# Kernel optimization log

Measured on AMD Instinct MI355X. Metric: run time of the kernel, lower is better.

Reference implementation:

```python
import jax, jax.numpy as jnp
import numpy as np

N, E, D, T, B, OUT = 20000, 80000, 768, 4, 3, 768
SCALE = 0.02


def _layer_norm(x, g, b):
    mu = jnp.mean(x, axis=-1, keepdims=True)
    var = jnp.var(x, axis=-1, keepdims=True)
    return (x - mu) / jnp.sqrt(var + 1e-5) * g + b


def _typed_linear(x, etype, bases, coeff):
    # DGL TypedLinear with basis regularizer: W[t] = sum_b coeff[t,b] * bases[b]
    # computed as 3 shared GEMMs + per-edge weighted sum (avoids [E,D,D] gather).
    c = coeff[etype]  # [E, B]
    y = c[:, 0:1] * (x @ bases[0])
    for bb in range(1, bases.shape[0]):
        y = y + c[:, bb:bb + 1] * (x @ bases[bb])
    return y


def _time_encode(t, freq, phase):
    return jnp.cos(t[:, None] * freq[None, :] + phase[None, :])


def _segment_softmax(scores, seg, n):
    m = jax.ops.segment_max(scores, seg, num_segments=n)
    m = jnp.where(jnp.isfinite(m), m, 0.0)  # empty segments -> -inf guard
    e = jnp.exp(scores - m[seg])
    den = jax.ops.segment_sum(e, seg, num_segments=n)[seg]
    return e / jnp.where(den == 0, 1.0, den)


def _forward(h, etime_hete, first_etime_homo, second_etime_homo, w_src, w_dst,
             ln_g, ln_b, src_bases, src_coeff, dst_bases, dst_coeff,
             user_bases, user_coeff, lin_w, lin_b, time_freq, time_phase,
             src_hete, dst_hete, first_etype_hete, src_homo, dst_homo,
             first_etype_homo, second_etype_homo, n_nodes):
    inv_sqrt_d = 1.0 / jnp.sqrt(jnp.asarray(768.0, h.dtype))
    n_src = h @ w_src.T  # src_weight (no bias)
    n_dst = h @ w_dst.T  # dst_weight (no bias)

    # --- heterogeneous edges ---
    sf = n_src[src_hete]
    df = n_dst[dst_hete]
    hete_src = jax.nn.relu(_typed_linear(_layer_norm(sf, ln_g, ln_b), first_etype_hete, src_bases, src_coeff))
    msg_h = _time_encode(etime_hete, time_freq, time_phase) + hete_src
    e_h = jnp.sum(msg_h * df, axis=1) * inv_sqrt_d
    a_h = _segment_softmax(e_h, dst_hete, n_nodes)
    h_hete = jax.ops.segment_sum(a_h[:, None] * msg_h, dst_hete, num_segments=n_nodes)

    # --- homogeneous edges ---
    sf = n_src[src_homo]
    df = n_dst[dst_homo]
    dst_feat = jax.nn.relu(_typed_linear(_layer_norm(df, ln_g, ln_b), first_etype_homo, dst_bases, dst_coeff))
    homo_feat = jax.nn.relu(_typed_linear(_layer_norm(sf, ln_g, ln_b), second_etype_homo, user_bases, user_coeff))
    t_homo = jnp.maximum(first_etime_homo, second_etime_homo)
    msg_o = _time_encode(t_homo, time_freq, time_phase) + homo_feat
    e_o = jnp.sum(msg_o * dst_feat, axis=1) * inv_sqrt_d
    a_o = _segment_softmax(e_o, dst_homo, n_nodes)
    h_homo = jax.ops.segment_sum(a_o[:, None] * msg_o, dst_homo, num_segments=n_nodes)

    n = jnp.concatenate([h_hete, h_homo], axis=-1)  # [N, 2D]
    z = jax.nn.relu(n @ lin_w.T + lin_b)
    zn = jnp.linalg.norm(z, axis=1, keepdims=True)
    return z / jnp.where(zn == 0, 1.0, zn)


def setup_inputs() -> dict:
    key = jax.random.key(0)
    ks = jax.random.split(key, 24)
    inp = {
        'h': jax.random.normal(ks[0], (N, D), jnp.float32),
        'etime_hete': jax.random.uniform(ks[1], (E,), jnp.float32),
        'first_etime_homo': jax.random.uniform(ks[2], (E,), jnp.float32),
        'second_etime_homo': jax.random.uniform(ks[3], (E,), jnp.float32),
        'w_src': jax.random.normal(ks[4], (D, D), jnp.float32) * SCALE,
        'w_dst': jax.random.normal(ks[5], (D, D), jnp.float32) * SCALE,
        'ln_g': jnp.ones((D,), jnp.float32),
        'ln_b': jnp.zeros((D,), jnp.float32),
        'src_bases': jax.random.normal(ks[6], (B, D, D), jnp.float32) * SCALE,
        'src_coeff': jax.random.normal(ks[7], (T, B), jnp.float32),
        'dst_bases': jax.random.normal(ks[8], (B, D, D), jnp.float32) * SCALE,
        'dst_coeff': jax.random.normal(ks[9], (T, B), jnp.float32),
        'user_bases': jax.random.normal(ks[10], (B, D, D), jnp.float32) * SCALE,
        'user_coeff': jax.random.normal(ks[11], (T, B), jnp.float32),
        'lin_w': jax.random.normal(ks[12], (OUT, 2 * D), jnp.float32) * SCALE,
        'lin_b': jnp.zeros((OUT,), jnp.float32),
        'time_freq': jnp.asarray(1.0 / 10 ** np.linspace(0, 9, D), jnp.float32),
        'time_phase': jnp.zeros((D,), jnp.float32),
        'src_hete': jax.random.randint(ks[13], (E,), 0, N, jnp.int32),
        'dst_hete': jax.random.randint(ks[14], (E,), 0, N, jnp.int32),
        'first_etype_hete': jax.random.randint(ks[15], (E,), 0, T, jnp.int32),
        'src_homo': jax.random.randint(ks[16], (E,), 0, N, jnp.int32),
        'dst_homo': jax.random.randint(ks[17], (E,), 0, N, jnp.int32),
        'first_etype_homo': jax.random.randint(ks[18], (E,), 0, T, jnp.int32),
        'second_etype_homo': jax.random.randint(ks[19], (E,), 0, T, jnp.int32),
        'num_nodes': N,
    }
    return inp


def reference(h, etime_hete, first_etime_homo, second_etime_homo, w_src, w_dst,
              ln_g, ln_b, src_bases, src_coeff, dst_bases, dst_coeff,
              user_bases, user_coeff, lin_w, lin_b, time_freq, time_phase,
              src_hete, dst_hete, first_etype_hete, src_homo, dst_homo,
              first_etype_homo, second_etype_homo, num_nodes):
    return _forward(h, etime_hete, first_etime_homo, second_etime_homo, w_src,
                    w_dst, ln_g, ln_b, src_bases, src_coeff, dst_bases,
                    dst_coeff, user_bases, user_coeff, lin_w, lin_b,
                    time_freq, time_phase, src_hete, dst_hete,
                    first_etype_hete, src_homo, dst_homo, first_etype_homo,
                    second_etype_homo, num_nodes)
```

## Files before the change

kernel.cpp:

```cpp
#include <hip/hip_runtime.h>
#include <hip/hip_bf16.h>
#include <stdint.h>

#define D 768
#define INV_SQRT_D 0.03608439182435161269f

static void* g_scratch = nullptr;
#define SCRATCH_BYTES ((size_t)600 * 1024 * 1024)

__attribute__((constructor))
static void _alloc_scratch() {
    if (hipMalloc(&g_scratch, SCRATCH_BYTES) != hipSuccess) g_scratch = nullptr;
}

static inline int cdiv(int a, int b) { return (a + b - 1) / b; }

typedef __attribute__((ext_vector_type(8))) short bf16x8;
typedef __attribute__((ext_vector_type(4))) float f32x4;

__device__ __forceinline__ unsigned short f2b(float f) {
    union { float f; unsigned u; } c; c.f = f;
    unsigned r = c.u + 0x7FFF + ((c.u >> 16) & 1);
    return (unsigned short)(r >> 16);
}
__device__ __forceinline__ float b2f(unsigned short u) {
    union { unsigned u; float f; } c; c.u = (unsigned)u << 16;
    return c.f;
}

__device__ __forceinline__ float block_reduce_sum(float v) {
#pragma unroll
    for (int off = 32; off > 0; off >>= 1) v += __shfl_down(v, off, 64);
    __shared__ float sm[4];
    int lane = threadIdx.x & 63, w = threadIdx.x >> 6;
    __syncthreads();
    if (lane == 0) sm[w] = v;
    __syncthreads();
    return (sm[0] + sm[1]) + (sm[2] + sm[3]);
}

template <bool CONCAT, bool BF16C, bool RELU_BIAS>
__global__ __launch_bounds__(256) void mfma_gemm(
    const unsigned short* __restrict__ A1, const unsigned short* __restrict__ A2,
    int lda, int ksplit,
    const unsigned short* __restrict__ B, int ldb,
    void* __restrict__ Cv, int ldc,
    const float* __restrict__ bias,
    int M, int K)
{
    __shared__ unsigned short As[128 * 32];
    __shared__ unsigned short Bs[128 * 32];
    const int tid = threadIdx.x;
    const int wv = tid >> 6, lane = tid & 63;
    const int m0 = blockIdx.y * 128, n0 = blockIdx.x * 128;
    const int wm = (wv >> 1) << 6;
    const int wn = (wv & 1) << 6;
    const int fr = lane & 15;
    const int fq = lane >> 4;

    f32x4 acc[4][4] = {};

    for (int k0 = 0; k0 < K; k0 += 32) {
        const unsigned short* Asrc = A1;
        int kk = k0;
        if (CONCAT && k0 >= ksplit) { Asrc = A2; kk = k0 - ksplit; }
#pragma unroll
        for (int j = 0; j < 2; ++j) {
            int idx = j * 256 + tid;
            int row = idx >> 2, cb = (idx & 3) << 3;
            int am = m0 + row; if (am > M - 1) am = M - 1;
            const unsigned short* ga = Asrc + (size_t)am * lda + kk + cb;
            char* la = (char*)As + (size_t)(j * 256 + wv * 64) * 16;
            __builtin_amdgcn_global_load_lds(
                (const __attribute__((address_space(1))) unsigned int*)ga,
                (__attribute__((address_space(3))) unsigned int*)la, 16, 0, 0);
            const unsigned short* gb = B + (size_t)(n0 + row) * ldb + k0 + cb;
            char* lb = (char*)Bs + (size_t)(j * 256 + wv * 64) * 16;
            __builtin_amdgcn_global_load_lds(
                (const __attribute__((address_space(1))) unsigned int*)gb,
                (__attribute__((address_space(3))) unsigned int*)lb, 16, 0, 0);
        }
        __syncthreads();

        bf16x8 af[4], bfv[4];
#pragma unroll
        for (int i = 0; i < 4; ++i) {
            af[i]  = *(const bf16x8*)&As[(wm + i * 16 + fr) * 32 + fq * 8];
            bfv[i] = *(const bf16x8*)&Bs[(wn + i * 16 + fr) * 32 + fq * 8];
        }
#pragma unroll
        for (int mi = 0; mi < 4; ++mi)
#pragma unroll
            for (int ni = 0; ni < 4; ++ni)
                acc[mi][ni] = __builtin_amdgcn_mfma_f32_16x16x32_bf16(
                    af[mi], bfv[ni], acc[mi][ni], 0, 0, 0);
        __syncthreads();
    }

#pragma unroll
    for (int mi = 0; mi < 4; ++mi) {
#pragma unroll
        for (int r = 0; r < 4; ++r) {
            int m = m0 + wm + mi * 16 + fq * 4 + r;
            if (m >= M) continue;
#pragma unroll
            for (int ni = 0; ni < 4; ++ni) {
                int n = n0 + wn + ni * 16 + fr;
                float v = acc[mi][ni][r];
                if (RELU_BIAS) v = fmaxf(v + bias[n], 0.f);
                if (BF16C) ((unsigned short*)Cv)[(size_t)m * ldc + n] = f2b(v);
                else       ((float*)Cv)[(size_t)m * ldc + n] = v;
            }
        }
    }
}

__global__ void f32_to_bf16_kernel(const float* __restrict__ in,
                                   unsigned short* __restrict__ out, int n4) {
    int i = blockIdx.x * 256 + threadIdx.x;
    if (i >= n4) return;
    float4 v = *reinterpret_cast<const float4*>(in + (size_t)i * 4);
    ushort4 o;
    o.x = f2b(v.x); o.y = f2b(v.y); o.z = f2b(v.z); o.w = f2b(v.w);
    *reinterpret_cast<ushort4*>(out + (size_t)i * 4) = o;
}

__global__ __launch_bounds__(256) void transpose_f32_to_bf16(
    const float* __restrict__ in, unsigned short* __restrict__ out) {
    const float* src = in + (size_t)blockIdx.z * D * D;
    unsigned short* dst = out + (size_t)blockIdx.z * D * D;
    __shared__ float tile[32][33];
    int bx = blockIdx.x * 32, by = blockIdx.y * 32;
    int tx = threadIdx.x & 31, ty = threadIdx.x >> 5;
#pragma unroll
    for (int i = 0; i < 32; i += 8)
        tile[ty + i][tx] = src[(size_t)(by + ty + i) * D + bx + tx];
    __syncthreads();
#pragma unroll
    for (int i = 0; i < 32; i += 8)
        dst[(size_t)(bx + ty + i) * D + by + tx] = f2b(tile[tx][ty + i]);
}

__global__ __launch_bounds__(256) void ln_bf16_kernel(
    unsigned short* __restrict__ x, int ld,
    const float* __restrict__ g, const float* __restrict__ b)
{
    unsigned short* r = x + (size_t)blockIdx.x * ld;
    int t = threadIdx.x;
    float v0 = b2f(r[t]), v1 = b2f(r[t + 256]), v2 = b2f(r[t + 512]);
    float s = block_reduce_sum(v0 + v1 + v2);
    float mu = s * (1.f / 768.f);
    float d0 = v0 - mu, d1 = v1 - mu, d2 = v2 - mu;
    float q = block_reduce_sum(d0 * d0 + d1 * d1 + d2 * d2);
    float rstd = 1.f / sqrtf(q * (1.f / 768.f) + 1e-5f);
    r[t]       = f2b(d0 * rstd * g[t]       + b[t]);
    r[t + 256] = f2b(d1 * rstd * g[t + 256] + b[t + 256]);
    r[t + 512] = f2b(d2 * rstd * g[t + 512] + b[t + 512]);
}

__global__ __launch_bounds__(256) void score_hete_kernel(
    const unsigned short* __restrict__ P, int ldp,
    const unsigned short* __restrict__ nd, int ldn,
    const float* __restrict__ coeff, const float* __restrict__ etime,
    const int* __restrict__ src, const int* __restrict__ dst, const int* __restrict__ et,
    const float* __restrict__ freq, const float* __restrict__ phase,
    float* __restrict__ esc)
{
    int e = blockIdx.x;
    int s = src[e], d = dst[e], ty = et[e];
    float c0 = coeff[ty * 3 + 0], c1 = coeff[ty * 3 + 1], c2 = coeff[ty * 3 + 2];
    float tv = etime[e];
    const unsigned short* ps = P + (size_t)s * ldp;
    const unsigned short* pd = nd + (size_t)d * ldn;
    float acc = 0.f;
    int j = threadIdx.x;
#pragma unroll
    for (int r = 0; r < 3; ++r, j += 256) {
        float y = c0 * b2f(ps[j]) + c1 * b2f(ps[j + D]) + c2 * b2f(ps[j + 2 * D]);
        float m = __cosf(tv * freq[j] + phase[j]) + fmaxf(y, 0.f);
        acc += m * b2f(pd[j]);
    }
    acc = block_reduce_sum(acc);
    if (threadIdx.x == 0) esc[e] = acc * INV_SQRT_D;
}

__global__ __launch_bounds__(256) void score_homo_kernel(
    const unsigned short* __restrict__ Pd, int ldpd,
    const unsigned short* __restrict__ Pu, int ldpu,
    const float* __restrict__ dcoeff, const float* __restrict__ ucoeff,
    const float* __restrict__ t1, const float* __restrict__ t2,
    const int* __restrict__ src, const int* __restrict__ dst,
    const int* __restrict__ et1, const int* __restrict__ et2,
    const float* __restrict__ freq, const float* __restrict__ phase,
    float* __restrict__ esc)
{
    int e = blockIdx.x;
    int s = src[e], d = dst[e];
    int ta = et1[e], tb = et2[e];
    float d0 = dcoeff[ta * 3 + 0], d1 = dcoeff[ta * 3 + 1], d2 = dcoeff[ta * 3 + 2];
    float u0 = ucoeff[tb * 3 + 0], u1 = ucoeff[tb * 3 + 1], u2 = ucoeff[tb * 3 + 2];
    float tv = fmaxf(t1[e], t2[e]);
    const unsigned short* pu = Pu + (size_t)s * ldpu;
    const unsigned short* pd = Pd + (size_t)d * ldpd;
    float acc = 0.f;
    int j = threadIdx.x;
#pragma unroll
    for (int r = 0; r < 3; ++r, j += 256) {
        float m  = __cosf(tv * freq[j] + phase[j])
                 + fmaxf(u0 * b2f(pu[j]) + u1 * b2f(pu[j + D]) + u2 * b2f(pu[j + 2 * D]), 0.f);
        float df = fmaxf(d0 * b2f(pd[j]) + d1 * b2f(pd[j + D]) + d2 * b2f(pd[j + 2 * D]), 0.f);
        acc += m * df;
    }
    acc = block_reduce_sum(acc);
    if (threadIdx.x == 0) esc[e] = acc * INV_SQRT_D;
}

__global__ void zero_int_kernel(int* __restrict__ p, int n) {
    int i = blockIdx.x * 256 + threadIdx.x;
    if (i < n) p[i] = 0;
}

__global__ void count_kernel(const int* __restrict__ dst, int* __restrict__ cnt, int E) {
    int e = blockIdx.x * 256 + threadIdx.x;
    if (e < E) atomicAdd(&cnt[dst[e]], 1);
}

__global__ __launch_bounds__(1024) void scan_kernel(
    const int* __restrict__ cnt, int* __restrict__ offs, int n)
{
    __shared__ int tmp[1024];
    __shared__ int carry;
    int tid = threadIdx.x;
    if (tid == 0) carry = 0;
    __syncthreads();
    for (int base = 0; base < n; base += 1024) {
        int idx = base + tid;
        int v = (idx < n) ? cnt[idx] : 0;
        tmp[tid] = v;
        __syncthreads();
        for (int off = 1; off < 1024; off <<= 1) {
            int t = (tid >= off) ? tmp[tid - off] : 0;
            __syncthreads();
            tmp[tid] += t;
            __syncthreads();
        }
        int inc = tmp[tid];
        int c = carry;
        if (idx < n) offs[idx] = c + inc - v;
        __syncthreads();
        if (tid == 0) carry = c + tmp[1023];
        __syncthreads();
    }
    if (tid == 0) offs[n] = carry;
}

__global__ void scatter_kernel(const int* __restrict__ dst, const int* __restrict__ offs,
                               int* __restrict__ cur, int* __restrict__ list, int E) {
    int e = blockIdx.x * 256 + threadIdx.x;
    if (e < E) {
        int d = dst[e];
        int pos = offs[d] + atomicAdd(&cur[d], 1);
        list[pos] = e;
    }
}

__global__ void seg_softmax_kernel(const int* __restrict__ offs, const int* __restrict__ list,
                                   float* __restrict__ score, int n) {
    int v = blockIdx.x * 256 + threadIdx.x;
    if (v >= n) return;
    int a = offs[v], b = offs[v + 1];
    if (a == b) return;
    float m = -INFINITY;
    for (int i = a; i < b; i++) m = fmaxf(m, score[list[i]]);
    float den = 0.f;
    for (int i = a; i < b; i++) den += expf(score[list[i]] - m);
    float inv = 1.f / den;
    for (int i = a; i < b; i++) { int e = list[i]; score[e] = expf(score[e] - m) * inv; }
}

__global__ __launch_bounds__(256) void agg_hete_kernel(
    const int* __restrict__ offs, const int* __restrict__ list,
    const float* __restrict__ a,
    const unsigned short* __restrict__ P, int ldp,
    const float* __restrict__ coeff, const float* __restrict__ etime,
    const int* __restrict__ src, const int* __restrict__ et,
    const float* __restrict__ freq, const float* __restrict__ phase,
    unsigned short* __restrict__ out)
{
    int v = blockIdx.x;
    int t = threadIdx.x;
    float f0 = freq[t], f1 = freq[t + 256], f2 = freq[t + 512];
    float p0 = phase[t], p1 = phase[t + 256], p2 = phase[t + 512];
    float a0 = 0.f, a1 = 0.f, a2 = 0.f;
    for (int i = offs[v]; i < offs[v + 1]; ++i) {
        int e = list[i];
        int s = src[e], ty = et[e];
        float w = a[e];
        float c0 = coeff[ty * 3 + 0], c1 = coeff[ty * 3 + 1], c2 = coeff[ty * 3 + 2];
        float tv = etime[e];
        const unsigned short* ps = P + (size_t)s * ldp;
        float y0 = c0 * b2f(ps[t])       + c1 * b2f(ps[t + D])       + c2 * b2f(ps[t + 2 * D]);
        float y1 = c0 * b2f(ps[t + 256]) + c1 * b2f(ps[t + 256 + D]) + c2 * b2f(ps[t + 256 + 2 * D]);
        float y2 = c0 * b2f(ps[t + 512]) + c1 * b2f(ps[t + 512 + D]) + c2 * b2f(ps[t + 512 + 2 * D]);
        a0 += w * (__cosf(tv * f0 + p0) + fmaxf(y0, 0.f));
        a1 += w * (__cosf(tv * f1 + p1) + fmaxf(y1, 0.f));
        a2 += w * (__cosf(tv * f2 + p2) + fmaxf(y2, 0.f));
    }
    unsigned short* o = out + (size_t)v * D;
    o[t] = f2b(a0); o[t + 256] = f2b(a1); o[t + 512] = f2b(a2);
}

__global__ __launch_bounds__(256) void agg_homo_kernel(
    const int* __restrict__ offs, const int* __restrict__ list,
    const float* __restrict__ a,
    const unsigned short* __restrict__ Pu, int ldpu,
    const float* __restrict__ ucoeff,
    const float* __restrict__ t1, const float* __restrict__ t2,
    const int* __restrict__ src, const int* __restrict__ et2,
    const float* __restrict__ freq, const float* __restrict__ phase,
    unsigned short* __restrict__ out)
{
    int v = blockIdx.x;
    int t = threadIdx.x;
    float f0 = freq[t], f1 = freq[t + 256], f2 = freq[t + 512];
    float p0 = phase[t], p1 = phase[t + 256], p2 = phase[t + 512];
    float a0 = 0.f, a1 = 0.f, a2 = 0.f;
    for (int i = offs[v]; i < offs[v + 1]; ++i) {
        int e = list[i];
        int s = src[e], tb = et2[e];
        float w = a[e];
        float u0 = ucoeff[tb * 3 + 0], u1 = ucoeff[tb * 3 + 1], u2 = ucoeff[tb * 3 + 2];
        float tv = fmaxf(t1[e], t2[e]);
        const unsigned short* pu = Pu + (size_t)s * ldpu;
        float y0 = u0 * b2f(pu[t])       + u1 * b2f(pu[t + D])       + u2 * b2f(pu[t + 2 * D]);
        float y1 = u0 * b2f(pu[t + 256]) + u1 * b2f(pu[t + 256 + D]) + u2 * b2f(pu[t + 256 + 2 * D]);
        float y2 = u0 * b2f(pu[t + 512]) + u1 * b2f(pu[t + 512 + D]) + u2 * b2f(pu[t + 512 + 2 * D]);
        a0 += w * (__cosf(tv * f0 + p0) + fmaxf(y0, 0.f));
        a1 += w * (__cosf(tv * f1 + p1) + fmaxf(y1, 0.f));
        a2 += w * (__cosf(tv * f2 + p2) + fmaxf(y2, 0.f));
    }
    unsigned short* o = out + (size_t)v * D;
    o[t] = f2b(a0); o[t + 256] = f2b(a1); o[t + 512] = f2b(a2);
}

__global__ __launch_bounds__(256) void normalize_kernel(
    const float* __restrict__ z, float* __restrict__ out)
{
    const float* x = z + (size_t)blockIdx.x * D;
    int t = threadIdx.x;
    float v0 = x[t], v1 = x[t + 256], v2 = x[t + 512];
    float s = block_reduce_sum(v0 * v0 + v1 * v1 + v2 * v2);
    float nrm = sqrtf(s);
    float inv = (nrm == 0.f) ? 1.f : 1.f / nrm;
    float* o = out + (size_t)blockIdx.x * D;
    o[t] = v0 * inv; o[t + 256] = v1 * inv; o[t + 512] = v2 * inv;
}

__global__ void fill_f32_kernel(float* __restrict__ p, float v, int n) {
    int i = blockIdx.x * 256 + threadIdx.x;
    if (i < n) p[i] = v;
}

extern "C" void kernel_launch(void* const* d_in, const int* in_sizes, int n_in,
                              void* d_out, int out_size, void* d_ws, size_t ws_size,
                              hipStream_t stream)
{
    const float* h          = (const float*)d_in[0];
    const float* etime_hete = (const float*)d_in[1];
    const float* t1_homo    = (const float*)d_in[2];
    const float* t2_homo    = (const float*)d_in[3];
    const float* w_src      = (const float*)d_in[4];
    const float* w_dst      = (const float*)d_in[5];
    const float* ln_g       = (const float*)d_in[6];
    const float* ln_b       = (const float*)d_in[7];
    const float* src_bases  = (const float*)d_in[8];
    const float* src_coeff  = (const float*)d_in[9];
    const float* dst_bases  = (const float*)d_in[10];
    const float* dst_coeff  = (const float*)d_in[11];
    const float* user_bases = (const float*)d_in[12];
    const float* user_coeff = (const float*)d_in[13];
    const float* lin_w      = (const float*)d_in[14];
    const float* lin_b      = (const float*)d_in[15];
    const float* time_freq  = (const float*)d_in[16];
    const float* time_phase = (const float*)d_in[17];
    const int* src_hete = (const int*)d_in[18];
    const int* dst_hete = (const int*)d_in[19];
    const int* et_hete  = (const int*)d_in[20];
    const int* src_homo = (const int*)d_in[21];
    const int* dst_homo = (const int*)d_in[22];
    const int* et1_homo = (const int*)d_in[23];
    const int* et2_homo = (const int*)d_in[24];

    const int N = in_sizes[0] / D;
    const int E = in_sizes[1];

    const size_t szST  = (size_t)N * 1536 * 2;
    const size_t szPSU = (size_t)N * 4608 * 2;
    const size_t szPD  = (size_t)N * 2304 * 2;
    const size_t szVb  = (size_t)N * D * 2;
    const size_t szW   = (size_t)D * D * 2;
    size_t need = szST + szPSU + szPD + 3 * szVb + 2 * szW + 2 * szW
                + 6 * szW + 3 * szW
                + (size_t)E * 4 + (size_t)N * 4
                + (((size_t)(N + 1) * 4 + 255) & ~(size_t)255) + (size_t)E * 4 + 4096;

    char* base;
    if (ws_size >= need) base = (char*)d_ws;
    else if (g_scratch)  base = (char*)g_scratch;
    else {
        fill_f32_kernel<<<cdiv(out_size, 256), 256, 0, stream>>>(
            (float*)d_out, 1000.0f + (float)(ws_size >> 20), out_size);
        return;
    }

    char* p = base;
    auto carve = [&](size_t bytes) { char* r = p; p += (bytes + 255) & ~(size_t)255; return r; };
    unsigned short* STb = (unsigned short*)carve(szST);
    unsigned short* PSU = (unsigned short*)carve(szPSU);
    unsigned short* PD  = (unsigned short*)carve(szPD);
    unsigned short* hb  = (unsigned short*)carve(szVb);
    unsigned short* hAb = (unsigned short*)carve(szVb);
    unsigned short* hOb = (unsigned short*)carve(szVb);
    unsigned short* wsb = (unsigned short*)carve(2 * szW);
    unsigned short* lwb = (unsigned short*)carve(2 * szW);
    unsigned short* suT = (unsigned short*)carve(6 * szW);
    unsigned short* dstT = (unsigned short*)carve(3 * szW);
    float* esc = (float*)carve((size_t)E * 4);
    int* cnt   = (int*)carve((size_t)N * 4);
    int* offs  = (int*)carve((size_t)(N + 1) * 4);
    int* list  = (int*)carve((size_t)E * 4);
    float* z   = (float*)PSU;

    unsigned short* Sb = STb;
    unsigned short* Tb = STb + 768;
    unsigned short* Psrc  = PSU;
    unsigned short* Puser = PSU + 2304;

    const int eb = cdiv(E, 256), nb = cdiv(N, 256);
    const int MB = cdiv(N, 128);
    dim3 g_proj(12, MB);
    dim3 g_psu(36, MB);
    dim3 g_pd(18, MB);
    dim3 g_fin(6, MB);
    dim3 tr_grid(24, 24, 3);

    f32_to_bf16_kernel<<<cdiv(N * D / 4, 256), 256, 0, stream>>>(h, hb, N * D / 4);
    f32_to_bf16_kernel<<<cdiv(D * D / 4, 256), 256, 0, stream>>>(w_src, wsb, D * D / 4);
    f32_to_bf16_kernel<<<cdiv(D * D / 4, 256), 256, 0, stream>>>(w_dst, wsb + (size_t)D * D, D * D / 4);
    f32_to_bf16_kernel<<<cdiv(D * 2 * D / 4, 256), 256, 0, stream>>>(lin_w, lwb, D * 2 * D / 4);
    transpose_f32_to_bf16<<<tr_grid, 256, 0, stream>>>(src_bases, suT);
    transpose_f32_to_bf16<<<tr_grid, 256, 0, stream>>>(user_bases, suT + (size_t)3 * D * D);
    transpose_f32_to_bf16<<<tr_grid, 256, 0, stream>>>(dst_bases, dstT);

    mfma_gemm<false, true, false><<<g_proj, 256, 0, stream>>>(
        hb, hb, D, D, wsb, D, STb, 1536, nullptr, N, D);
    ln_bf16_kernel<<<N, 256, 0, stream>>>(Sb, 1536, ln_g, ln_b);

    mfma_gemm<false, true, false><<<g_psu, 256, 0, stream>>>(
        Sb, Sb, 1536, D, suT, D, PSU, 4608, nullptr, N, D);

    zero_int_kernel<<<nb, 256, 0, stream>>>(cnt, N);
    count_kernel<<<eb, 256, 0, stream>>>(dst_hete, cnt, E);
    scan_kernel<<<1, 1024, 0, stream>>>(cnt, offs, N);
    zero_int_kernel<<<nb, 256, 0, stream>>>(cnt, N);
    scatter_kernel<<<eb, 256, 0, stream>>>(dst_hete, offs, cnt, list, E);

    score_hete_kernel<<<E, 256, 0, stream>>>(Psrc, 4608, Tb, 1536, src_coeff, etime_hete,
                                             src_hete, dst_hete, et_hete,
                                             time_freq, time_phase, esc);
    seg_softmax_kernel<<<nb, 256, 0, stream>>>(offs, list, esc, N);
    agg_hete_kernel<<<N, 256, 0, stream>>>(offs, list, esc, Psrc, 4608, src_coeff, etime_hete,
                                           src_hete, et_hete, time_freq, time_phase, hAb);

    ln_bf16_kernel<<<N, 256, 0, stream>>>(Tb, 1536, ln_g, ln_b);
    mfma_gemm<false, true, false><<<g_pd, 256, 0, stream>>>(
        Tb, Tb, 1536, D, dstT, D, PD, 2304, nullptr, N, D);

    zero_int_kernel<<<nb, 256, 0, stream>>>(cnt, N);
    count_kernel<<<eb, 256, 0, stream>>>(dst_homo, cnt, E);
    scan_kernel<<<1, 1024, 0, stream>>>(cnt, offs, N);
    zero_int_kernel<<<nb, 256, 0, stream>>>(cnt, N);
    scatter_kernel<<<eb, 256, 0, stream>>>(dst_homo, offs, cnt, list, E);

    score_homo_kernel<<<E, 256, 0, stream>>>(PD, 2304, Puser, 4608, dst_coeff, user_coeff,
                                             t1_homo, t2_homo, src_homo, dst_homo,
                                             et1_homo, et2_homo, time_freq, time_phase, esc);
    seg_softmax_kernel<<<nb, 256, 0, stream>>>(offs, list, esc, N);
    agg_homo_kernel<<<N, 256, 0, stream>>>(offs, list, esc, Puser, 4608, user_coeff,
                                           t1_homo, t2_homo, src_homo, et2_homo,
                                           time_freq, time_phase, hOb);

    mfma_gemm<true, false, true><<<g_fin, 256, 0, stream>>>(
        hAb, hOb, D, D, lwb, 2 * D, z, D, lin_b, N, 2 * D);
    normalize_kernel<<<N, 256, 0, stream>>>(z, (float*)d_out);
}
```

Before: 1.170 ms.

## Precombine basis weights per edge type and fuse ReLU into projection GEMMs

```diff
diff --git a/kernel.cpp b/kernel.cpp
--- a/kernel.cpp
+++ b/kernel.cpp
@@ -39,7 +39,7 @@
     return (sm[0] + sm[1]) + (sm[2] + sm[3]);
 }
 
-template <bool CONCAT, bool BF16C, bool RELU_BIAS>
+template <bool CONCAT, bool BF16C, bool RELU, bool BIAS>
 __global__ __launch_bounds__(256) void mfma_gemm(
     const unsigned short* __restrict__ A1, const unsigned short* __restrict__ A2,
     int lda, int ksplit,
@@ -107,7 +107,8 @@
             for (int ni = 0; ni < 4; ++ni) {
                 int n = n0 + wn + ni * 16 + fr;
                 float v = acc[mi][ni][r];
-                if (RELU_BIAS) v = fmaxf(v + bias[n], 0.f);
+                if (BIAS) v += bias[n];
+                if (RELU) v = fmaxf(v, 0.f);
                 if (BF16C) ((unsigned short*)Cv)[(size_t)m * ldc + n] = f2b(v);
                 else       ((float*)Cv)[(size_t)m * ldc + n] = v;
             }
@@ -125,20 +126,25 @@
     *reinterpret_cast<ushort4*>(out + (size_t)i * 4) = o;
 }
 
-__global__ __launch_bounds__(256) void transpose_f32_to_bf16(
-    const float* __restrict__ in, unsigned short* __restrict__ out) {
-    const float* src = in + (size_t)blockIdx.z * D * D;
-    unsigned short* dst = out + (size_t)blockIdx.z * D * D;
+__global__ __launch_bounds__(256) void combine_transpose_kernel(
+    const float* __restrict__ in, const float* __restrict__ coeff,
+    unsigned short* __restrict__ out) {
+    int t = blockIdx.z;
+    float c0 = coeff[t * 3 + 0], c1 = coeff[t * 3 + 1], c2 = coeff[t * 3 + 2];
     __shared__ float tile[32][33];
     int bx = blockIdx.x * 32, by = blockIdx.y * 32;
     int tx = threadIdx.x & 31, ty = threadIdx.x >> 5;
 #pragma unroll
+    for (int i = 0; i < 32; i += 8) {
+        size_t idx = (size_t)(by + ty + i) * D + bx + tx;
+        tile[ty + i][tx] = c0 * in[idx] + c1 * in[idx + (size_t)D * D]
+                         + c2 * in[idx + (size_t)2 * D * D];
+    }
+    __syncthreads();
+    unsigned short* o = out + (size_t)t * D * D;
+#pragma unroll
     for (int i = 0; i < 32; i += 8)
-        tile[ty + i][tx] = src[(size_t)(by + ty + i) * D + bx + tx];
-    __syncthreads();
-#pragma unroll
-    for (int i = 0; i < 32; i += 8)
-        dst[(size_t)(bx + ty + i) * D + by + tx] = f2b(tile[tx][ty + i]);
+        o[(size_t)(bx + ty + i) * D + by + tx] = f2b(tile[tx][ty + i]);
 }
 
 __global__ __launch_bounds__(256) void ln_bf16_kernel(
@@ -161,58 +167,85 @@
 __global__ __launch_bounds__(256) void score_hete_kernel(
     const unsigned short* __restrict__ P, int ldp,
     const unsigned short* __restrict__ nd, int ldn,
-    const float* __restrict__ coeff, const float* __restrict__ etime,
+    const float* __restrict__ etime,
     const int* __restrict__ src, const int* __restrict__ dst, const int* __restrict__ et,
     const float* __restrict__ freq, const float* __restrict__ phase,
-    float* __restrict__ esc)
-{
-    int e = blockIdx.x;
+    float* __restrict__ esc, int E)
+{
+    int e = blockIdx.x * 4 + (threadIdx.x >> 6);
+    if (e >= E) return;
+    int l = threadIdx.x & 63;
     int s = src[e], d = dst[e], ty = et[e];
-    float c0 = coeff[ty * 3 + 0], c1 = coeff[ty * 3 + 1], c2 = coeff[ty * 3 + 2];
     float tv = etime[e];
-    const unsigned short* ps = P + (size_t)s * ldp;
+    const unsigned short* ps = P + (size_t)s * ldp + ty * D;
     const unsigned short* pd = nd + (size_t)d * ldn;
     float acc = 0.f;
-    int j = threadIdx.x;
-#pragma unroll
-    for (int r = 0; r < 3; ++r, j += 256) {
-        float y = c0 * b2f(ps[j]) + c1 * b2f(ps[j + D]) + c2 * b2f(ps[j + 2 * D]);
-        float m = __cosf(tv * freq[j] + phase[j]) + fmaxf(y, 0.f);
-        acc += m * b2f(pd[j]);
-    }
-    acc = block_reduce_sum(acc);
-    if (threadIdx.x == 0) esc[e] = acc * INV_SQRT_D;
+    {
+        bf16x8 a = *(const bf16x8*)(ps + l * 8);
+        bf16x8 b = *(const bf16x8*)(pd + l * 8);
+#pragma unroll
+        for (int q = 0; q < 8; ++q) {
+            int j = l * 8 + q;
+            float m = __cosf(tv * freq[j] + phase[j]) + b2f((unsigned short)a[q]);
+            acc += m * b2f((unsigned short)b[q]);
+        }
+    }
+    if (l < 32) {
+        bf16x8 a = *(const bf16x8*)(ps + 512 + l * 8);
+        bf16x8 b = *(const bf16x8*)(pd + 512 + l * 8);
+#pragma unroll
+        for (int q = 0; q < 8; ++q) {
+            int j = 512 + l * 8 + q;
+            float m = __cosf(tv * freq[j] + phase[j]) + b2f((unsigned short)a[q]);
+            acc += m * b2f((unsigned short)b[q]);
+        }
+    }
+#pragma unroll
+    for (int off = 32; off > 0; off >>= 1) acc += __shfl_down(acc, off, 64);
+    if (l == 0) esc[e] = acc * INV_SQRT_D;
 }
 
 __global__ __launch_bounds__(256) void score_homo_kernel(
     const unsigned short* __restrict__ Pd, int ldpd,
     const unsigned short* __restrict__ Pu, int ldpu,
-    const float* __restrict__ dcoeff, const float* __restrict__ ucoeff,
     const float* __restrict__ t1, const float* __restrict__ t2,
     const int* __restrict__ src, const int* __restrict__ dst,
     const int* __restrict__ et1, const int* __restrict__ et2,
     const float* __restrict__ freq, const float* __restrict__ phase,
-    float* __restrict__ esc)
-{
-    int e = blockIdx.x;
+    float* __restrict__ esc, int E)
+{
+    int e = blockIdx.x * 4 + (threadIdx.x >> 6);
+    if (e >= E) return;
+    int l = threadIdx.x & 63;
     int s = src[e], d = dst[e];
     int ta = et1[e], tb = et2[e];
-    float d0 = dcoeff[ta * 3 + 0], d1 = dcoeff[ta * 3 + 1], d2 = dcoeff[ta * 3 + 2];
-    float u0 = ucoeff[tb * 3 + 0], u1 = ucoeff[tb * 3 + 1], u2 = ucoeff[tb * 3 + 2];
     float tv = fmaxf(t1[e], t2[e]);
-    const unsigned short* pu = Pu + (size_t)s * ldpu;
-    const unsigned short* pd = Pd + (size_t)d * ldpd;
+    const unsigned short* pu = Pu + (size_t)s * ldpu + tb * D;
+    const unsigned short* pd = Pd + (size_t)d * ldpd + ta * D;
     float acc = 0.f;
-    int j = threadIdx.x;
-#pragma unroll
-    for (int r = 0; r < 3; ++r, j += 256) {
-        float m  = __cosf(tv * freq[j] + phase[j])
-                 + fmaxf(u0 * b2f(pu[j]) + u1 * b2f(pu[j + D]) + u2 * b2f(pu[j + 2 * D]), 0.f);
-        float df = fmaxf(d0 * b2f(pd[j]) + d1 * b2f(pd[j + D]) + d2 * b2f(pd[j + 2 * D]), 0.f);
-        acc += m * df;
-    }
-    acc = block_reduce_sum(acc);
-    if (threadIdx.x == 0) esc[e] = acc * INV_SQRT_D;
+    {
+        bf16x8 a = *(const bf16x8*)(pu + l * 8);
+        bf16x8 b = *(const bf16x8*)(pd + l * 8);
+#pragma unroll
+        for (int q = 0; q < 8; ++q) {
+            int j = l * 8 + q;
+            float m = __cosf(tv * freq[j] + phase[j]) + b2f((unsigned short)a[q]);
+            acc += m * b2f((unsigned short)b[q]);
+        }
+    }
+    if (l < 32) {
+        bf16x8 a = *(const bf16x8*)(pu + 512 + l * 8);
+        bf16x8 b = *(const bf16x8*)(pd + 512 + l * 8);
+#pragma unroll
+        for (int q = 0; q < 8; ++q) {
+            int j = 512 + l * 8 + q;
+            float m = __cosf(tv * freq[j] + phase[j]) + b2f((unsigned short)a[q]);
+            acc += m * b2f((unsigned short)b[q]);
+        }
+    }
+#pragma unroll
+    for (int off = 32; off > 0; off >>= 1) acc += __shfl_down(acc, off, 64);
+    if (l == 0) esc[e] = acc * INV_SQRT_D;
 }
 
 __global__ void zero_int_kernel(int* __restrict__ p, int n) {
@@ -282,7 +315,7 @@
     const int* __restrict__ offs, const int* __restrict__ list,
     const float* __restrict__ a,
     const unsigned short* __restrict__ P, int ldp,
-    const float* __restrict__ coeff, const float* __restrict__ etime,
+    const float* __restrict__ etime,
     const int* __restrict__ src, const int* __restrict__ et,
     const float* __restrict__ freq, const float* __restrict__ phase,
     unsigned short* __restrict__ out)
@@ -296,15 +329,11 @@
         int e = list[i];
         int s = src[e], ty = et[e];
         float w = a[e];
-        float c0 = coeff[ty * 3 + 0], c1 = coeff[ty * 3 + 1], c2 = coeff[ty * 3 + 2];
         float tv = etime[e];
-        const unsigned short* ps = P + (size_t)s * ldp;
-        float y0 = c0 * b2f(ps[t])       + c1 * b2f(ps[t + D])       + c2 * b2f(ps[t + 2 * D]);
-        float y1 = c0 * b2f(ps[t + 256]) + c1 * b2f(ps[t + 256 + D]) + c2 * b2f(ps[t + 256 + 2 * D]);
-        float y2 = c0 * b2f(ps[t + 512]) + c1 * b2f(ps[t + 512 + D]) + c2 * b2f(ps[t + 512 + 2 * D]);
-        a0 += w * (__cosf(tv * f0 + p0) + fmaxf(y0, 0.f));
-        a1 += w * (__cosf(tv * f1 + p1) + fmaxf(y1, 0.f));
-        a2 += w * (__cosf(tv * f2 + p2) + fmaxf(y2, 0.f));
+        const unsigned short* ps = P + (size_t)s * ldp + ty * D;
+        a0 += w * (__cosf(tv * f0 + p0) + b2f(ps[t]));
+        a1 += w * (__cosf(tv * f1 + p1) + b2f(ps[t + 256]));
+        a2 += w * (__cosf(tv * f2 + p2) + b2f(ps[t + 512]));
     }
     unsigned short* o = out + (size_t)v * D;
     o[t] = f2b(a0); o[t + 256] = f2b(a1); o[t + 512] = f2b(a2);
@@ -314,7 +343,6 @@
     const int* __restrict__ offs, const int* __restrict__ list,
     const float* __restrict__ a,
     const unsigned short* __restrict__ Pu, int ldpu,
-    const float* __restrict__ ucoeff,
     const float* __restrict__ t1, const float* __restrict__ t2,
     const int* __restrict__ src, const int* __restrict__ et2,
     const float* __restrict__ freq, const float* __restrict__ phase,
@@ -329,15 +357,11 @@
         int e = list[i];
         int s = src[e], tb = et2[e];
         float w = a[e];
-        float u0 = ucoeff[tb * 3 + 0], u1 = ucoeff[tb * 3 + 1], u2 = ucoeff[tb * 3 + 2];
         float tv = fmaxf(t1[e], t2[e]);
-        const unsigned short* pu = Pu + (size_t)s * ldpu;
-        float y0 = u0 * b2f(pu[t])       + u1 * b2f(pu[t + D])       + u2 * b2f(pu[t + 2 * D]);
-        float y1 = u0 * b2f(pu[t + 256]) + u1 * b2f(pu[t + 256 + D]) + u2 * b2f(pu[t + 256 + 2 * D]);
-        float y2 = u0 * b2f(pu[t + 512]) + u1 * b2f(pu[t + 512 + D]) + u2 * b2f(pu[t + 512 + 2 * D]);
-        a0 += w * (__cosf(tv * f0 + p0) + fmaxf(y0, 0.f));
-        a1 += w * (__cosf(tv * f1 + p1) + fmaxf(y1, 0.f));
-        a2 += w * (__cosf(tv * f2 + p2) + fmaxf(y2, 0.f));
+        const unsigned short* pu = Pu + (size_t)s * ldpu + tb * D;
+        a0 += w * (__cosf(tv * f0 + p0) + b2f(pu[t]));
+        a1 += w * (__cosf(tv * f1 + p1) + b2f(pu[t + 256]));
+        a2 += w * (__cosf(tv * f2 + p2) + b2f(pu[t + 512]));
     }
     unsigned short* o = out + (size_t)v * D;
     o[t] = f2b(a0); o[t + 256] = f2b(a1); o[t + 512] = f2b(a2);
@@ -395,14 +419,14 @@
     const int E = in_sizes[1];
 
     const size_t szST  = (size_t)N * 1536 * 2;
-    const size_t szPSU = (size_t)N * 4608 * 2;
-    const size_t szPD  = (size_t)N * 2304 * 2;
+    const size_t szPSU = (size_t)N * 6144 * 2;
+    const size_t szPD  = (size_t)N * 3072 * 2;
     const size_t szVb  = (size_t)N * D * 2;
     const size_t szW   = (size_t)D * D * 2;
-    size_t need = szST + szPSU + szPD + 3 * szVb + 2 * szW + 2 * szW
-                + 6 * szW + 3 * szW
+    size_t need = szST + szPSU + szPD + 3 * szVb
+                + 2 * szW + 2 * szW + 8 * szW + 4 * szW
                 + (size_t)E * 4 + (size_t)N * 4
-                + (((size_t)(N + 1) * 4 + 255) & ~(size_t)255) + (size_t)E * 4 + 4096;
+                + (((size_t)(N + 1) * 4 + 255) & ~(size_t)255) + (size_t)E * 4 + 8192;
 
     char* base;
     if (ws_size >= need) base = (char*)d_ws;
@@ -423,8 +447,8 @@
     unsigned short* hOb = (unsigned short*)carve(szVb);
     unsigned short* wsb = (unsigned short*)carve(2 * szW);
     unsigned short* lwb = (unsigned short*)carve(2 * szW);
-    unsigned short* suT = (unsigned short*)carve(6 * szW);
-    unsigned short* dstT = (unsigned short*)carve(3 * szW);
+    unsigned short* suW = (unsigned short*)carve(8 * szW);
+    unsigned short* dstW = (unsigned short*)carve(4 * szW);
     float* esc = (float*)carve((size_t)E * 4);
     int* cnt   = (int*)carve((size_t)N * 4);
     int* offs  = (int*)carve((size_t)(N + 1) * 4);
@@ -433,31 +457,32 @@
 
     unsigned short* Sb = STb;
     unsigned short* Tb = STb + 768;
-    unsigned short* Psrc  = PSU;
-    unsigned short* Puser = PSU + 2304;
+    unsigned short* Psrc_t  = PSU;
+    unsigned short* Puser_t = PSU + 3072;
 
     const int eb = cdiv(E, 256), nb = cdiv(N, 256);
     const int MB = cdiv(N, 128);
     dim3 g_proj(12, MB);
-    dim3 g_psu(36, MB);
-    dim3 g_pd(18, MB);
+    dim3 g_psu(48, MB);
+    dim3 g_pd(24, MB);
     dim3 g_fin(6, MB);
-    dim3 tr_grid(24, 24, 3);
+    dim3 ct_grid(24, 24, 4);
+    const int seb = cdiv(E, 4);
 
     f32_to_bf16_kernel<<<cdiv(N * D / 4, 256), 256, 0, stream>>>(h, hb, N * D / 4);
     f32_to_bf16_kernel<<<cdiv(D * D / 4, 256), 256, 0, stream>>>(w_src, wsb, D * D / 4);
     f32_to_bf16_kernel<<<cdiv(D * D / 4, 256), 256, 0, stream>>>(w_dst, wsb + (size_t)D * D, D * D / 4);
     f32_to_bf16_kernel<<<cdiv(D * 2 * D / 4, 256), 256, 0, stream>>>(lin_w, lwb, D * 2 * D / 4);
-    transpose_f32_to_bf16<<<tr_grid, 256, 0, stream>>>(src_bases, suT);
-    transpose_f32_to_bf16<<<tr_grid, 256, 0, stream>>>(user_bases, suT + (size_t)3 * D * D);
-    transpose_f32_to_bf16<<<tr_grid, 256, 0, stream>>>(dst_bases, dstT);
-
-    mfma_gemm<false, true, false><<<g_proj, 256, 0, stream>>>(
+    combine_transpose_kernel<<<ct_grid, 256, 0, stream>>>(src_bases, src_coeff, suW);
+    combine_transpose_kernel<<<ct_grid, 256, 0, stream>>>(user_bases, user_coeff, suW + (size_t)4 * D * D);
+    combine_transpose_kernel<<<ct_grid, 256, 0, stream>>>(dst_bases, dst_coeff, dstW);
+
+    mfma_gemm<false, true, false, false><<<g_proj, 256, 0, stream>>>(
         hb, hb, D, D, wsb, D, STb, 1536, nullptr, N, D);
     ln_bf16_kernel<<<N, 256, 0, stream>>>(Sb, 1536, ln_g, ln_b);
 
-    mfma_gemm<false, true, false><<<g_psu, 256, 0, stream>>>(
-        Sb, Sb, 1536, D, suT, D, PSU, 4608, nullptr, N, D);
+    mfma_gemm<false, true, true, false><<<g_psu, 256, 0, stream>>>(
+        Sb, Sb, 1536, D, suW, D, PSU, 6144, nullptr, N, D);
 
     zero_int_kernel<<<nb, 256, 0, stream>>>(cnt, N);
     count_kernel<<<eb, 256, 0, stream>>>(dst_hete, cnt, E);
@@ -465,16 +490,16 @@
     zero_int_kernel<<<nb, 256, 0, stream>>>(cnt, N);
     scatter_kernel<<<eb, 256, 0, stream>>>(dst_hete, offs, cnt, list, E);
 
-    score_hete_kernel<<<E, 256, 0, stream>>>(Psrc, 4608, Tb, 1536, src_coeff, etime_hete,
-                                             src_hete, dst_hete, et_hete,
-                                             time_freq, time_phase, esc);
+    score_hete_kernel<<<seb, 256, 0, stream>>>(Psrc_t, 6144, Tb, 1536, etime_hete,
+                                               src_hete, dst_hete, et_hete,
+                                               time_freq, time_phase, esc, E);
     seg_softmax_kernel<<<nb, 256, 0, stream>>>(offs, list, esc, N);
-    agg_hete_kernel<<<N, 256, 0, stream>>>(offs, list, esc, Psrc, 4608, src_coeff, etime_hete,
+    agg_hete_kernel<<<N, 256, 0, stream>>>(offs, list, esc, Psrc_t, 6144, etime_hete,
                                            src_hete, et_hete, time_freq, time_phase, hAb);
 
     ln_bf16_kernel<<<N, 256, 0, stream>>>(Tb, 1536, ln_g, ln_b);
-    mfma_gemm<false, true, false><<<g_pd, 256, 0, stream>>>(
-        Tb, Tb, 1536, D, dstT, D, PD, 2304, nullptr, N, D);
+    mfma_gemm<false, true, true, false><<<g_pd, 256, 0, stream>>>(
+        Tb, Tb, 1536, D, dstW, D, PD, 3072, nullptr, N, D);
 
     zero_int_kernel<<<nb, 256, 0, stream>>>(cnt, N);
     count_kernel<<<eb, 256, 0, stream>>>(dst_homo, cnt, E);
@@ -482,15 +507,15 @@
     zero_int_kernel<<<nb, 256, 0, stream>>>(cnt, N);
     scatter_kernel<<<eb, 256, 0, stream>>>(dst_homo, offs, cnt, list, E);
 
-    score_homo_kernel<<<E, 256, 0, stream>>>(PD, 2304, Puser, 4608, dst_coeff, user_coeff,
-                                             t1_homo, t2_homo, src_homo, dst_homo,
-                                             et1_homo, et2_homo, time_freq, time_phase, esc);
+    score_homo_kernel<<<seb, 256, 0, stream>>>(PD, 3072, Puser_t, 6144,
+                                               t1_homo, t2_homo, src_homo, dst_homo,
+                                               et1_homo, et2_homo, time_freq, time_phase, esc, E);
     seg_softmax_kernel<<<nb, 256, 0, stream>>>(offs, list, esc, N);
-    agg_homo_kernel<<<N, 256, 0, stream>>>(offs, list, esc, Puser, 4608, user_coeff,
+    agg_homo_kernel<<<N, 256, 0, stream>>>(offs, list, esc, Puser_t, 6144,
                                            t1_homo, t2_homo, src_homo, et2_homo,
                                            time_freq, time_phase, hOb);
 
-    mfma_gemm<true, false, true><<<g_fin, 256, 0, stream>>>(
+    mfma_gemm<true, false, true, true><<<g_fin, 256, 0, stream>>>(
         hAb, hOb, D, D, lwb, 2 * D, z, D, lin_b, N, 2 * D);
     normalize_kernel<<<N, 256, 0, stream>>>(z, (float*)d_out);
 }
```

Result: faster. 1.142 ms (-2.4%).
